# Performance work log

Measured on AMD Instinct MI355X. Metric: run time of the kernel, lower is better.

The kernel has to match this reference:

```python
import jax, jax.numpy as jnp
import numpy as np

RNN = 64      # rnn_hidden_dim
HID = 64      # hidden_dim
ENC = 3       # encoder_dim
NAG = 8       # n_agents
NACT = 14     # n_actions
CLIP = 0.2    # args.exp_clip (variance floor)
BN_EPS = 1e-5


def _bn(x, g, b):
    # BatchNorm1d in training mode: batch stats, biased variance
    m = x.mean(0)
    v = jnp.mean((x - m) ** 2, 0)
    return g * (x - m) * jax.lax.rsqrt(v + BN_EPS) + b


def setup_inputs() -> dict:
    key = jax.random.key(0)
    ks = jax.random.split(key, 16)
    B, INP = 8192, 96

    def w(k, shape, fan):
        return (jax.random.normal(k, shape, jnp.float32) / np.float32(np.sqrt(fan)))

    d = {}
    d["inputs"] = jax.random.normal(ks[0], (B * NAG, INP), jnp.float32)
    d["hidden_state"] = jax.random.normal(ks[1], (B * NAG, RNN), jnp.float32)
    d["noise"] = jax.random.normal(ks[2], (B, NAG, NAG * ENC), jnp.float32)
    d["fc1_w"] = w(ks[3], (INP, RNN), INP); d["fc1_b"] = jnp.zeros((RNN,), jnp.float32)
    d["w_ih"] = w(ks[4], (RNN, 3 * RNN), RNN); d["w_hh"] = w(ks[5], (RNN, 3 * RNN), RNN)
    d["b_ih"] = jnp.zeros((3 * RNN,), jnp.float32); d["b_hh"] = jnp.zeros((3 * RNN,), jnp.float32)
    d["aw1_w"] = w(ks[6], (RNN, HID), RNN); d["aw1_b"] = jnp.zeros((HID,), jnp.float32)
    d["aw_g"] = jnp.ones((HID,), jnp.float32); d["aw_be"] = jnp.zeros((HID,), jnp.float32)
    d["aw2_w"] = w(ks[7], (HID, 2 * NAG * ENC), HID); d["aw2_b"] = jnp.zeros((2 * NAG * ENC,), jnp.float32)
    d["po1_w"] = w(ks[8], (2 * RNN, HID), 2 * RNN); d["po1_b"] = jnp.zeros((HID,), jnp.float32)
    d["po_g"] = jnp.ones((HID,), jnp.float32); d["po_be"] = jnp.zeros((HID,), jnp.float32)
    d["po2_w"] = w(ks[9], (HID, 2 * ENC), HID); d["po2_b"] = jnp.zeros((2 * ENC,), jnp.float32)
    d["fc2_w"] = w(ks[10], (RNN + ENC * NAG, NACT), RNN + ENC * NAG); d["fc2_b"] = jnp.zeros((NACT,), jnp.float32)
    return d


def reference(inputs, hidden_state, noise,
              fc1_w, fc1_b, w_ih, w_hh, b_ih, b_hh,
              aw1_w, aw1_b, aw_g, aw_be, aw2_w, aw2_b,
              po1_w, po1_b, po_g, po_be, po2_w, po2_b,
              fc2_w, fc2_b):
    B, n, enc = noise.shape[0], NAG, ENC

    x = jax.nn.relu(inputs @ fc1_w + fc1_b)                      # [B*n, RNN]
    h_in = hidden_state.reshape(-1, RNN)

    # torch GRUCell
    gi = x @ w_ih + b_ih
    gh = h_in @ w_hh + b_hh
    ir, iz, i_n = jnp.split(gi, 3, axis=-1)
    hr, hz, h_n = jnp.split(gh, 3, axis=-1)
    r = jax.nn.sigmoid(ir + hr)
    z = jax.nn.sigmoid(iz + hz)
    nt = jnp.tanh(i_n + r * h_n)
    h = (1.0 - z) * nt + z * h_in                                # [B*n, RNN]

    # awareness encoder
    a = jax.nn.relu(_bn(h @ aw1_w + aw1_b, aw_g, aw_be))
    aw = (a @ aw2_w + aw2_b).reshape(B, n, 2 * n * enc)
    mu = aw[:, :, : n * enc]
    sigma = jnp.maximum(jnp.exp(aw[:, :, n * enc:]), CLIP)       # variance
    c = (mu + jnp.sqrt(sigma) * noise).reshape(-1, n * enc)      # rsample

    x_out = jnp.concatenate([h, c], axis=-1) @ fc2_w + fc2_b     # [B*n, NACT]

    # poster branch (training mode): all-pairs concat H[b, j, id] = [h[b,id], h[b,j]]
    hd = jax.lax.stop_gradient(h).reshape(B, n, RNN)
    Hi = jnp.broadcast_to(hd[:, None, :, :], (B, n, n, RNN))     # axis2 = id
    Hj = jnp.broadcast_to(hd[:, :, None, :], (B, n, n, RNN))     # axis1 = j
    H = jnp.concatenate([Hi, Hj], axis=-1).reshape(-1, 2 * RNN)  # [B*n*n, 2*RNN]

    p = jax.nn.relu(_bn(H @ po1_w + po1_b, po_g, po_be))
    out = (p @ po2_w + po2_b).reshape(B, n, 2 * n * enc)
    mu1 = out[:, :, : n * enc]
    sigma1 = jnp.maximum(jnp.exp(out[:, :, n * enc:]), CLIP)

    # KL between diagonal Gaussians (sigma, sigma1 are variances)
    kl = 0.5 * (jnp.log(sigma1 / sigma) + (sigma + (mu - mu1) ** 2) / sigma1 - 1.0)
    KL = kl.mean(axis=-1).mean(axis=-1, keepdims=True)           # [B, 1]
    return (x_out, h, KL)
```

## Files before the change

### kernel.cpp

```cpp
#include <hip/hip_runtime.h>
#include <math.h>

#define NROWS 65536
#define NB    8192
#define STAT_OFF  0
#define DERIV_OFF 448
#define WPACK_OFF 1088
#define OUT_XOUT 0
#define OUT_H    917504
#define OUT_KL   5111808

typedef __attribute__((ext_vector_type(8))) short bhalf8;
typedef __attribute__((ext_vector_type(4))) float floatx4;
typedef __attribute__((ext_vector_type(4))) unsigned short u16x4;

__device__ __forceinline__ float sigmf(float x) { return 1.0f / (1.0f + __expf(-x)); }
__device__ __forceinline__ float tanhfast(float x) {
    x = fminf(fmaxf(x, -15.f), 15.f);
    float e = __expf(-2.f * x);
    return (1.f - e) / (1.f + e);
}
__device__ __forceinline__ unsigned short f2bf(float f) {
    unsigned int u = __float_as_uint(f);
    u += 0x7FFFu + ((u >> 16) & 1u);
    return (unsigned short)(u >> 16);
}
__device__ __forceinline__ float bf2f(unsigned short s) {
    return __uint_as_float(((unsigned int)s) << 16);
}

__global__ void k_prep(const float* __restrict__ fc1_w,
                       const float* __restrict__ w_ih, const float* __restrict__ w_hh,
                       const float* __restrict__ aw1_w, const float* __restrict__ po1_w,
                       const float* __restrict__ aw2_w, const float* __restrict__ fc2_w,
                       float* __restrict__ ws)
{
    const int t = threadIdx.x;
    if (blockIdx.x == 0)
        for (int i = t; i < 448; i += 256) ws[STAT_OFF + i] = 0.f;

    unsigned short* wpk = (unsigned short*)(ws + WPACK_OFF);
    for (int f = blockIdx.x * 256 + t; f < 5952; f += gridDim.x * 256) {
        int lane, c, tile;
        const float* src;
        int colbase, krowstride, kofs, kmax = 1 << 30, colmax = 16;
        if (f < 768) {
            tile = f / 192; c = (f % 192) / 64; lane = f % 64;
            src = fc1_w; krowstride = 64; colbase = tile * 16; kofs = 0;
        } else if (f < 3840) {
            int f2 = f - 768;
            tile = f2 / 128; c = (f2 % 128) / 64; lane = f2 % 64;
            if (tile < 12) { src = w_ih; colbase = tile * 16; }
            else           { src = w_hh; colbase = (tile - 12) * 16; }
            krowstride = 192; kofs = 0;
        } else if (f < 5376) {
            int f3 = f - 3840;
            tile = f3 / 128; c = (f3 % 128) / 64; lane = f3 % 64;
            if (tile < 4)       { src = aw1_w; colbase = tile * 16; kofs = 0; }
            else if (tile < 8)  { src = po1_w; colbase = (tile - 4) * 16; kofs = 0; }
            else                { src = po1_w; colbase = (tile - 8) * 16; kofs = 64; }
            krowstride = 64;
        } else if (f < 5760) {
            int f4 = f - 5376;
            tile = f4 / 128; c = (f4 % 128) / 64; lane = f4 % 64;
            src = aw2_w; krowstride = 48; colbase = tile * 16; kofs = 0;
        } else {
            int f5 = f - 5760;
            c = f5 / 64; lane = f5 % 64;
            src = fc2_w; krowstride = 14; colbase = 0; kofs = 0;
            kmax = 88; colmax = 14;
        }
        int n = lane & 15, quad = lane >> 4;
        int col = colbase + n;
        unsigned short o[8];
        #pragma unroll
        for (int j = 0; j < 8; j++) {
            int k = c * 32 + quad * 8 + j + kofs;
            float v = (k < kmax && n < colmax) ? src[(size_t)k * krowstride + col] : 0.f;
            o[j] = f2bf(v);
        }
        u16x4 lo, hi;
        lo.x = o[0]; lo.y = o[1]; lo.z = o[2]; lo.w = o[3];
        hi.x = o[4]; hi.y = o[5]; hi.z = o[6]; hi.w = o[7];
        *(u16x4*)&wpk[f * 8]     = lo;
        *(u16x4*)&wpk[f * 8 + 4] = hi;
    }
}

__global__ __launch_bounds__(256) void k_front(
    const float* __restrict__ inp, const float* __restrict__ hin,
    const float* __restrict__ fc1_b,
    const float* __restrict__ b_ih, const float* __restrict__ b_hh,
    const float* __restrict__ aw1_b,
    float* __restrict__ h_out, float* __restrict__ ws)
{
    __shared__ __align__(16) unsigned short s_inpb[64 * 104];
    __shared__ __align__(16) unsigned short s_hinb[64 * 88];
    __shared__ __align__(16) unsigned short s_xb[64 * 88];
    __shared__ float s_stat[448];

    const int t = threadIdx.x;
    const int row0 = blockIdx.x * 64;
    const int lane = t & 63;
    const int w = t >> 6;
    const int n16 = lane & 15;
    const int quad = lane >> 4;
    const int mrow = w * 16 + n16;

    {
        const float* gi = inp + (size_t)row0 * 96;
        for (int i = t; i < 1536; i += 256) {
            int r = i / 24, c4 = (i - r * 24) * 4;
            float4 v = *(const float4*)&gi[r * 96 + c4];
            u16x4 p; p.x = f2bf(v.x); p.y = f2bf(v.y); p.z = f2bf(v.z); p.w = f2bf(v.w);
            *(u16x4*)&s_inpb[r * 104 + c4] = p;
        }
        const float* gh = hin + (size_t)row0 * 64;
        for (int i = t; i < 1024; i += 256) {
            int r = i >> 4, c4 = (i & 15) * 4;
            float4 v = *(const float4*)&gh[r * 64 + c4];
            u16x4 p; p.x = f2bf(v.x); p.y = f2bf(v.y); p.z = f2bf(v.z); p.w = f2bf(v.w);
            *(u16x4*)&s_hinb[r * 88 + c4] = p;
        }
    }
    for (int i = t; i < 448; i += 256) s_stat[i] = 0.f;
    __syncthreads();

    const bhalf8* wp1 = (const bhalf8*)((const unsigned short*)(ws + WPACK_OFF));
    const bhalf8* wp2 = wp1 + 768;
    const bhalf8* wp3 = wp1 + 3840;

    {
        bhalf8 ai0 = *(const bhalf8*)&s_inpb[mrow * 104 + 0  + quad * 8];
        bhalf8 ai1 = *(const bhalf8*)&s_inpb[mrow * 104 + 32 + quad * 8];
        bhalf8 ai2 = *(const bhalf8*)&s_inpb[mrow * 104 + 64 + quad * 8];
        #pragma unroll
        for (int g = 0; g < 4; g++) {
            floatx4 d = {0.f, 0.f, 0.f, 0.f};
            d = __builtin_amdgcn_mfma_f32_16x16x32_bf16(ai0, wp1[(g * 3 + 0) * 64 + lane], d, 0, 0, 0);
            d = __builtin_amdgcn_mfma_f32_16x16x32_bf16(ai1, wp1[(g * 3 + 1) * 64 + lane], d, 0, 0, 0);
            d = __builtin_amdgcn_mfma_f32_16x16x32_bf16(ai2, wp1[(g * 3 + 2) * 64 + lane], d, 0, 0, 0);
            int col = g * 16 + n16;
            float bb = fc1_b[col];
            #pragma unroll
            for (int q = 0; q < 4; q++) {
                float xv = fmaxf(d[q] + bb, 0.f);
                s_xb[(w * 16 + quad * 4 + q) * 88 + col] = f2bf(xv);
            }
        }
    }

    floatx4 gr[4], gz[4], gn[4], gh2[4];
    {
        bhalf8 ax0 = *(const bhalf8*)&s_xb[mrow * 88 + 0  + quad * 8];
        bhalf8 ax1 = *(const bhalf8*)&s_xb[mrow * 88 + 32 + quad * 8];
        bhalf8 ah0 = *(const bhalf8*)&s_hinb[mrow * 88 + 0  + quad * 8];
        bhalf8 ah1 = *(const bhalf8*)&s_hinb[mrow * 88 + 32 + quad * 8];
        #pragma unroll
        for (int g = 0; g < 4; g++) {
            floatx4 d = {0.f, 0.f, 0.f, 0.f};
            d = __builtin_amdgcn_mfma_f32_16x16x32_bf16(ax0, wp2[((0 + g) * 2 + 0) * 64 + lane], d, 0, 0, 0);
            d = __builtin_amdgcn_mfma_f32_16x16x32_bf16(ax1, wp2[((0 + g) * 2 + 1) * 64 + lane], d, 0, 0, 0);
            d = __builtin_amdgcn_mfma_f32_16x16x32_bf16(ah0, wp2[((12 + g) * 2 + 0) * 64 + lane], d, 0, 0, 0);
            d = __builtin_amdgcn_mfma_f32_16x16x32_bf16(ah1, wp2[((12 + g) * 2 + 1) * 64 + lane], d, 0, 0, 0);
            gr[g] = d;
            floatx4 e = {0.f, 0.f, 0.f, 0.f};
            e = __builtin_amdgcn_mfma_f32_16x16x32_bf16(ax0, wp2[((4 + g) * 2 + 0) * 64 + lane], e, 0, 0, 0);
            e = __builtin_amdgcn_mfma_f32_16x16x32_bf16(ax1, wp2[((4 + g) * 2 + 1) * 64 + lane], e, 0, 0, 0);
            e = __builtin_amdgcn_mfma_f32_16x16x32_bf16(ah0, wp2[((16 + g) * 2 + 0) * 64 + lane], e, 0, 0, 0);
            e = __builtin_amdgcn_mfma_f32_16x16x32_bf16(ah1, wp2[((16 + g) * 2 + 1) * 64 + lane], e, 0, 0, 0);
            gz[g] = e;
            floatx4 p = {0.f, 0.f, 0.f, 0.f};
            p = __builtin_amdgcn_mfma_f32_16x16x32_bf16(ax0, wp2[((8 + g) * 2 + 0) * 64 + lane], p, 0, 0, 0);
            p = __builtin_amdgcn_mfma_f32_16x16x32_bf16(ax1, wp2[((8 + g) * 2 + 1) * 64 + lane], p, 0, 0, 0);
            gn[g] = p;
            floatx4 s = {0.f, 0.f, 0.f, 0.f};
            s = __builtin_amdgcn_mfma_f32_16x16x32_bf16(ah0, wp2[((20 + g) * 2 + 0) * 64 + lane], s, 0, 0, 0);
            s = __builtin_amdgcn_mfma_f32_16x16x32_bf16(ah1, wp2[((20 + g) * 2 + 1) * 64 + lane], s, 0, 0, 0);
            gh2[g] = s;
        }
    }
    __syncthreads();

    unsigned short* s_hb = s_inpb;
    #pragma unroll
    for (int g = 0; g < 4; g++) {
        int col = g * 16 + n16;
        float br_ = b_ih[col] + b_hh[col];
        float bz_ = b_ih[64 + col] + b_hh[64 + col];
        float bin_ = b_ih[128 + col];
        float bhn_ = b_hh[128 + col];
        #pragma unroll
        for (int q = 0; q < 4; q++) {
            int lrow = w * 16 + quad * 4 + q;
            size_t grow = (size_t)(row0 + lrow);
            float r  = sigmf(gr[g][q] + br_);
            float z  = sigmf(gz[g][q] + bz_);
            float nt = tanhfast(gn[g][q] + bin_ + r * (gh2[g][q] + bhn_));
            float hp = hin[grow * 64 + col];
            float h  = (1.f - z) * nt + z * hp;
            h_out[grow * 64 + col] = h;
            s_hb[lrow * 88 + col] = f2bf(h);
        }
    }

    {
        bhalf8 ah0 = *(const bhalf8*)&s_hb[mrow * 88 + 0  + quad * 8];
        bhalf8 ah1 = *(const bhalf8*)&s_hb[mrow * 88 + 32 + quad * 8];
        floatx4 g3[12];
        #pragma unroll
        for (int tt = 0; tt < 12; tt++) {
            floatx4 d = {0.f, 0.f, 0.f, 0.f};
            d = __builtin_amdgcn_mfma_f32_16x16x32_bf16(ah0, wp3[(tt * 2 + 0) * 64 + lane], d, 0, 0, 0);
            d = __builtin_amdgcn_mfma_f32_16x16x32_bf16(ah1, wp3[(tt * 2 + 1) * 64 + lane], d, 0, 0, 0);
            g3[tt] = d;
        }
        #pragma unroll
        for (int g = 0; g < 4; g++) {
            int col = g * 16 + n16;
            float ab = aw1_b[col];
            float s1 = 0.f, s2 = 0.f;
            #pragma unroll
            for (int q = 0; q < 4; q++) {
                float v = g3[g][q] + ab;
                s1 += v; s2 += v * v;
            }
            float t1 = s1 + __shfl_xor(s1, 16, 64); t1 += __shfl_xor(t1, 32, 64);
            float t2 = s2 + __shfl_xor(s2, 16, 64); t2 += __shfl_xor(t2, 32, 64);
            if (quad == 0) {
                atomicAdd(&s_stat[col], t1);
                atomicAdd(&s_stat[64 + col], t2);
            }
        }
        #pragma unroll
        for (int g = 0; g < 4; g++) {
            int col = g * 16 + n16;
            float su = 0.f, suq = 0.f, sv = 0.f, svq = 0.f;
            #pragma unroll
            for (int q = 0; q < 4; q++) {
                float uv = g3[4 + g][q]; su += uv; suq += uv * uv;
                float vv = g3[8 + g][q]; sv += vv; svq += vv * vv;
            }
            float u8 = su + __shfl_xor(su, 16, 64);
            float v8 = sv + __shfl_xor(sv, 16, 64);
            if ((quad & 1) == 0)
                atomicAdd(&s_stat[384 + col], u8 * v8 * (1.f / 64.f));
            float su16 = u8 + __shfl_xor(u8, 32, 64);
            float sv16 = v8 + __shfl_xor(v8, 32, 64);
            float suq16 = suq + __shfl_xor(suq, 16, 64); suq16 += __shfl_xor(suq16, 32, 64);
            float svq16 = svq + __shfl_xor(svq, 16, 64); svq16 += __shfl_xor(svq16, 32, 64);
            if (quad == 0) {
                atomicAdd(&s_stat[128 + col], su16);
                atomicAdd(&s_stat[192 + col], suq16);
                atomicAdd(&s_stat[256 + col], sv16);
                atomicAdd(&s_stat[320 + col], svq16);
            }
        }
    }
    __syncthreads();
    if (t < 64) {
        float* gs = ws + STAT_OFF;
        #pragma unroll
        for (int q = 0; q < 7; q++)
            atomicAdd(&gs[q * 64 + t], s_stat[q * 64 + t]);
    }
}

__global__ void k_stats(const float* __restrict__ aw_g, const float* __restrict__ aw_be,
                        const float* __restrict__ po_g, const float* __restrict__ po_be,
                        const float* __restrict__ po1_b, const float* __restrict__ po2_w,
                        float* __restrict__ ws)
{
    const int t = threadIdx.x;
    const float* st = ws + STAT_OFF;
    float* dv = ws + DERIV_OFF;
    if (t < 64) {
        const float invN = 1.f / 65536.f;
        float am = st[t] * invN;
        float av = st[64 + t] * invN - am * am;
        float asc = aw_g[t] * rsqrtf(av + 1e-5f);
        dv[t] = asc;
        dv[64 + t] = aw_be[t] - asc * am;
        float Eu = st[128 + t] * invN;
        float vu = st[192 + t] * invN - Eu * Eu;
        float Ev = st[256 + t] * invN;
        float vv = st[320 + t] * invN - Ev * Ev;
        float cov = st[384 + t] * (1.f / 8192.f) - Eu * Ev;
        float my = Eu + Ev + po1_b[t];
        float vy = vu + vv + 2.f * cov;
        float psc = po_g[t] * rsqrtf(vy + 1e-5f);
        dv[128 + t] = psc;
        dv[192 + t] = po_be[t] + psc * (po1_b[t] - my);
    }
    for (int i = t; i < 384; i += 128) {
        int d = i >> 6, c = i & 63;
        dv[256 + i] = po2_w[c * 6 + d];
    }
}

__global__ __launch_bounds__(128) void k_heads(
    const float* __restrict__ h_glob, const float* __restrict__ noise,
    const float* __restrict__ aw1_b, const float* __restrict__ aw2_b,
    const float* __restrict__ fc2_b, const float* __restrict__ po2_b,
    const float* __restrict__ ws, float* __restrict__ out)
{
    __shared__ __align__(16) unsigned short s_hb[32 * 104];
    __shared__ __align__(16) unsigned short s_U[32 * 72];
    __shared__ __align__(16) unsigned short s_V[32 * 72];
    __shared__ float s_ms[32 * 48];
    __shared__ __align__(16) float s_u2[32 * 48];
    __shared__ float s_kl[32];

    const int t = threadIdx.x;
    const int row0 = blockIdx.x * 32;
    const int b0 = blockIdx.x * 4;
    const int lane = t & 63;
    const int w = t >> 6;
    const int n16 = lane & 15;
    const int quad = lane >> 4;
    const int mrow = w * 16 + n16;
    const float* dv = ws + DERIV_OFF;

    {
        const float* gh = h_glob + (size_t)row0 * 64;
        for (int i = t; i < 512; i += 128) {
            int r = i >> 4, c4 = (i & 15) * 4;
            float4 v = *(const float4*)&gh[r * 64 + c4];
            u16x4 p; p.x = f2bf(v.x); p.y = f2bf(v.y); p.z = f2bf(v.z); p.w = f2bf(v.w);
            *(u16x4*)&s_hb[r * 104 + c4] = p;
        }
        for (int i = t; i < 64; i += 128) {
            int r = i >> 1, c4 = 88 + (i & 1) * 4;
            u16x4 z; z.x = 0; z.y = 0; z.z = 0; z.w = 0;
            *(u16x4*)&s_hb[r * 104 + c4] = z;
        }
    }
    __syncthreads();

    const bhalf8* wp3  = ((const bhalf8*)((const unsigned short*)(ws + WPACK_OFF))) + 3840;
    const bhalf8* wpa2 = wp3 + 1536;
    const bhalf8* wpf2 = wpa2 + 384;
    unsigned short* s_ab = (unsigned short*)s_u2;

    {
        bhalf8 ah0 = *(const bhalf8*)&s_hb[mrow * 104 + 0  + quad * 8];
        bhalf8 ah1 = *(const bhalf8*)&s_hb[mrow * 104 + 32 + quad * 8];
        floatx4 g3[12];
        #pragma unroll
        for (int tt = 0; tt < 12; tt++) {
            floatx4 d = {0.f, 0.f, 0.f, 0.f};
            d = __builtin_amdgcn_mfma_f32_16x16x32_bf16(ah0, wp3[(tt * 2 + 0) * 64 + lane], d, 0, 0, 0);
            d = __builtin_amdgcn_mfma_f32_16x16x32_bf16(ah1, wp3[(tt * 2 + 1) * 64 + lane], d, 0, 0, 0);
            g3[tt] = d;
        }
        #pragma unroll
        for (int g = 0; g < 4; g++) {
            int col = g * 16 + n16;
            float ab = aw1_b[col];
            float sc = dv[col], sf = dv[64 + col];
            #pragma unroll
            for (int q = 0; q < 4; q++) {
                int lrow = w * 16 + quad * 4 + q;
                float a = fmaxf(sc * (g3[g][q] + ab) + sf, 0.f);
                s_ab[lrow * 72 + col] = f2bf(a);
                s_U[lrow * 72 + col] = f2bf(g3[4 + g][q]);
                s_V[lrow * 72 + col] = f2bf(g3[8 + g][q]);
            }
        }
    }
    __syncthreads();

    {
        bhalf8 aa0 = *(const bhalf8*)&s_ab[mrow * 72 + 0  + quad * 8];
        bhalf8 aa1 = *(const bhalf8*)&s_ab[mrow * 72 + 32 + quad * 8];
        #pragma unroll
        for (int g = 0; g < 3; g++) {
            floatx4 d = {0.f, 0.f, 0.f, 0.f};
            d = __builtin_amdgcn_mfma_f32_16x16x32_bf16(aa0, wpa2[(g * 2 + 0) * 64 + lane], d, 0, 0, 0);
            d = __builtin_amdgcn_mfma_f32_16x16x32_bf16(aa1, wpa2[(g * 2 + 1) * 64 + lane], d, 0, 0, 0);
            int col = g * 16 + n16;
            float bb = aw2_b[col];
            #pragma unroll
            for (int q = 0; q < 4; q++) {
                int lrow = w * 16 + quad * 4 + q;
                float v = d[q] + bb;
                s_ms[lrow * 48 + col] = (col < 24) ? v : fmaxf(__expf(v), 0.2f);
            }
        }
    }
    __syncthreads();

    for (int i = t; i < 768; i += 128) {
        int r = i / 24, m = i - r * 24;
        float c = s_ms[r * 48 + m] + sqrtf(s_ms[r * 48 + 24 + m]) * noise[(size_t)(row0 + r) * 24 + m];
        s_hb[r * 104 + 64 + m] = f2bf(c);
    }
    __syncthreads();

    {
        bhalf8 hc0 = *(const bhalf8*)&s_hb[mrow * 104 + 0  + quad * 8];
        bhalf8 hc1 = *(const bhalf8*)&s_hb[mrow * 104 + 32 + quad * 8];
        bhalf8 hc2 = *(const bhalf8*)&s_hb[mrow * 104 + 64 + quad * 8];
        floatx4 d = {0.f, 0.f, 0.f, 0.f};
        d = __builtin_amdgcn_mfma_f32_16x16x32_bf16(hc0, wpf2[0 * 64 + lane], d, 0, 0, 0);
        d = __builtin_amdgcn_mfma_f32_16x16x32_bf16(hc1, wpf2[1 * 64 + lane], d, 0, 0, 0);
        d = __builtin_amdgcn_mfma_f32_16x16x32_bf16(hc2, wpf2[2 * 64 + lane], d, 0, 0, 0);
        if (n16 < 14) {
            float bb = fc2_b[n16];
            float* xout = out + OUT_XOUT;
            #pragma unroll
            for (int q = 0; q < 4; q++) {
                size_t grow = (size_t)(row0 + w * 16 + quad * 4 + q);
                xout[grow * 14 + n16] = d[q] + bb;
            }
        }
    }
    __syncthreads();

    float* s_out = s_u2;
    {
        const float* psc = dv + 128;
        const float* psh = dv + 192;
        const float* p2t = dv + 256;
        const int bl = t >> 5;
        const int rem = t & 31;
        const int i_ = rem >> 2;
        const int j0 = (rem & 3) * 2;
        float acc[2][6];
        #pragma unroll
        for (int jj = 0; jj < 2; jj++)
            #pragma unroll
            for (int d = 0; d < 6; d++) acc[jj][d] = 0.f;

        for (int c = 0; c < 64; c += 4) {
            u16x4 vb = *(const u16x4*)&s_V[(bl * 8 + i_) * 72 + c];
            float vv[4] = {bf2f(vb.x), bf2f(vb.y), bf2f(vb.z), bf2f(vb.w)};
            float ps[4]; *(float4*)ps = *(const float4*)&psc[c];
            float pf[4]; *(float4*)pf = *(const float4*)&psh[c];
            float wv[6][4];
            #pragma unroll
            for (int d = 0; d < 6; d++) *(float4*)wv[d] = *(const float4*)&p2t[d * 64 + c];
            #pragma unroll
            for (int jj = 0; jj < 2; jj++) {
                u16x4 ub = *(const u16x4*)&s_U[(bl * 8 + j0 + jj) * 72 + c];
                float p[4];
                p[0] = fmaxf(ps[0] * (bf2f(ub.x) + vv[0]) + pf[0], 0.f);
                p[1] = fmaxf(ps[1] * (bf2f(ub.y) + vv[1]) + pf[1], 0.f);
                p[2] = fmaxf(ps[2] * (bf2f(ub.z) + vv[2]) + pf[2], 0.f);
                p[3] = fmaxf(ps[3] * (bf2f(ub.w) + vv[3]) + pf[3], 0.f);
                #pragma unroll
                for (int d = 0; d < 6; d++)
                    acc[jj][d] += p[0] * wv[d][0] + p[1] * wv[d][1] + p[2] * wv[d][2] + p[3] * wv[d][3];
            }
        }
        #pragma unroll
        for (int jj = 0; jj < 2; jj++)
            #pragma unroll
            for (int d = 0; d < 6; d++)
                s_out[(bl * 8 + i_) * 48 + (j0 + jj) * 6 + d] = acc[jj][d] + po2_b[d];
    }
    __syncthreads();

    if (t < 32) {
        float s = 0.f;
        #pragma unroll 4
        for (int m = 0; m < 24; m++) {
            float mu0 = s_ms[t * 48 + m];
            float sg0 = s_ms[t * 48 + 24 + m];
            float mu1 = s_out[t * 48 + m];
            float sg1 = fmaxf(__expf(s_out[t * 48 + 24 + m]), 0.2f);
            float d0 = mu0 - mu1;
            s += __logf(sg1 / sg0) + (sg0 + d0 * d0) / sg1 - 1.f;
        }
        s_kl[t] = s;
    }
    __syncthreads();
    if (t < 4) {
        float s = 0.f;
        #pragma unroll
        for (int i = 0; i < 8; i++) s += s_kl[t * 8 + i];
        out[OUT_KL + b0 + t] = s * (0.5f / 192.f);
    }
}

extern "C" void kernel_launch(void* const* d_in, const int* in_sizes, int n_in,
                              void* d_out, int out_size, void* d_ws, size_t ws_size,
                              hipStream_t stream)
{
    (void)in_sizes; (void)n_in; (void)out_size; (void)ws_size;
    const float* inp   = (const float*)d_in[0];
    const float* hin   = (const float*)d_in[1];
    const float* noise = (const float*)d_in[2];
    const float* fc1_w = (const float*)d_in[3];
    const float* fc1_b = (const float*)d_in[4];
    const float* w_ih  = (const float*)d_in[5];
    const float* w_hh  = (const float*)d_in[6];
    const float* b_ih  = (const float*)d_in[7];
    const float* b_hh  = (const float*)d_in[8];
    const float* aw1_w = (const float*)d_in[9];
    const float* aw1_b = (const float*)d_in[10];
    const float* aw_g  = (const float*)d_in[11];
    const float* aw_be = (const float*)d_in[12];
    const float* aw2_w = (const float*)d_in[13];
    const float* aw2_b = (const float*)d_in[14];
    const float* po1_w = (const float*)d_in[15];
    const float* po1_b = (const float*)d_in[16];
    const float* po_g  = (const float*)d_in[17];
    const float* po_be = (const float*)d_in[18];
    const float* po2_w = (const float*)d_in[19];
    const float* po2_b = (const float*)d_in[20];
    const float* fc2_w = (const float*)d_in[21];
    const float* fc2_b = (const float*)d_in[22];
    float* out = (float*)d_out;
    float* ws  = (float*)d_ws;

    hipLaunchKernelGGL(k_prep,  dim3(8),    dim3(256), 0, stream,
                       fc1_w, w_ih, w_hh, aw1_w, po1_w, aw2_w, fc2_w, ws);
    hipLaunchKernelGGL(k_front, dim3(1024), dim3(256), 0, stream,
                       inp, hin, fc1_b, b_ih, b_hh, aw1_b, out + OUT_H, ws);
    hipLaunchKernelGGL(k_stats, dim3(1),    dim3(128), 0, stream,
                       aw_g, aw_be, po_g, po_be, po1_b, po2_w, ws);
    hipLaunchKernelGGL(k_heads, dim3(2048), dim3(128), 0, stream,
                       out + OUT_H, noise, aw1_b, aw2_b, fc2_b, po2_b, ws, out);
}
```

Before: 211.5 us.

## Double rows per front block, fold stats kernel into heads, prescale U/V in fp32

k_front now handles 128 rows per block, so each wave computes two 16-row MFMA tiles that share every loaded weight fragment, which halves weight fragment loads per row and the number of blocks. The single-block k_stats launch is removed, and each k_heads block recomputes the BatchNorm-derived scale and shift into shared memory, saving a serialized launch at the cost of redundant per-block work. The poster U/V terms are stored in fp32 with the BN scale and shift already applied, which cuts multiply work in the all-pairs loop but enlarges shared memory. k_prep uses more blocks, and the per-tile stat reductions are merged to issue fewer shuffles and atomics.

```diff
diff --git a/kernel.cpp b/kernel.cpp
--- a/kernel.cpp
+++ b/kernel.cpp
@@ -4,8 +4,7 @@
 #define NROWS 65536
 #define NB    8192
 #define STAT_OFF  0
-#define DERIV_OFF 448
-#define WPACK_OFF 1088
+#define WPACK_OFF 448
 #define OUT_XOUT 0
 #define OUT_H    917504
 #define OUT_KL   5111808
@@ -25,9 +24,6 @@
     u += 0x7FFFu + ((u >> 16) & 1u);
     return (unsigned short)(u >> 16);
 }
-__device__ __forceinline__ float bf2f(unsigned short s) {
-    return __uint_as_float(((unsigned int)s) << 16);
-}
 
 __global__ void k_prep(const float* __restrict__ fc1_w,
                        const float* __restrict__ w_ih, const float* __restrict__ w_hh,
@@ -43,31 +39,31 @@
     for (int f = blockIdx.x * 256 + t; f < 5952; f += gridDim.x * 256) {
         int lane, c, tile;
         const float* src;
-        int colbase, krowstride, kofs, kmax = 1 << 30, colmax = 16;
+        int colbase, krowstride, kofs = 0, kmax = 1 << 30, colmax = 16;
         if (f < 768) {
             tile = f / 192; c = (f % 192) / 64; lane = f % 64;
-            src = fc1_w; krowstride = 64; colbase = tile * 16; kofs = 0;
+            src = fc1_w; krowstride = 64; colbase = tile * 16;
         } else if (f < 3840) {
             int f2 = f - 768;
             tile = f2 / 128; c = (f2 % 128) / 64; lane = f2 % 64;
             if (tile < 12) { src = w_ih; colbase = tile * 16; }
             else           { src = w_hh; colbase = (tile - 12) * 16; }
-            krowstride = 192; kofs = 0;
+            krowstride = 192;
         } else if (f < 5376) {
             int f3 = f - 3840;
             tile = f3 / 128; c = (f3 % 128) / 64; lane = f3 % 64;
-            if (tile < 4)       { src = aw1_w; colbase = tile * 16; kofs = 0; }
-            else if (tile < 8)  { src = po1_w; colbase = (tile - 4) * 16; kofs = 0; }
+            if (tile < 4)       { src = aw1_w; colbase = tile * 16; }
+            else if (tile < 8)  { src = po1_w; colbase = (tile - 4) * 16; }
             else                { src = po1_w; colbase = (tile - 8) * 16; kofs = 64; }
             krowstride = 64;
         } else if (f < 5760) {
             int f4 = f - 5376;
             tile = f4 / 128; c = (f4 % 128) / 64; lane = f4 % 64;
-            src = aw2_w; krowstride = 48; colbase = tile * 16; kofs = 0;
+            src = aw2_w; krowstride = 48; colbase = tile * 16;
         } else {
             int f5 = f - 5760;
             c = f5 / 64; lane = f5 % 64;
-            src = fc2_w; krowstride = 14; colbase = 0; kofs = 0;
+            src = fc2_w; krowstride = 14; colbase = 0;
             kmax = 88; colmax = 14;
         }
         int n = lane & 15, quad = lane >> 4;
@@ -87,36 +83,35 @@
     }
 }
 
-__global__ __launch_bounds__(256) void k_front(
+__global__ __launch_bounds__(256, 2) void k_front(
     const float* __restrict__ inp, const float* __restrict__ hin,
     const float* __restrict__ fc1_b,
     const float* __restrict__ b_ih, const float* __restrict__ b_hh,
     const float* __restrict__ aw1_b,
     float* __restrict__ h_out, float* __restrict__ ws)
 {
-    __shared__ __align__(16) unsigned short s_inpb[64 * 104];
-    __shared__ __align__(16) unsigned short s_hinb[64 * 88];
-    __shared__ __align__(16) unsigned short s_xb[64 * 88];
+    __shared__ __align__(16) unsigned short s_inpb[128 * 104];
+    __shared__ __align__(16) unsigned short s_hinb[128 * 88];
+    __shared__ __align__(16) unsigned short s_xb[128 * 88];
     __shared__ float s_stat[448];
 
     const int t = threadIdx.x;
-    const int row0 = blockIdx.x * 64;
+    const int row0 = blockIdx.x * 128;
     const int lane = t & 63;
     const int w = t >> 6;
     const int n16 = lane & 15;
     const int quad = lane >> 4;
-    const int mrow = w * 16 + n16;
 
     {
         const float* gi = inp + (size_t)row0 * 96;
-        for (int i = t; i < 1536; i += 256) {
+        for (int i = t; i < 3072; i += 256) {
             int r = i / 24, c4 = (i - r * 24) * 4;
             float4 v = *(const float4*)&gi[r * 96 + c4];
             u16x4 p; p.x = f2bf(v.x); p.y = f2bf(v.y); p.z = f2bf(v.z); p.w = f2bf(v.w);
             *(u16x4*)&s_inpb[r * 104 + c4] = p;
         }
         const float* gh = hin + (size_t)row0 * 64;
-        for (int i = t; i < 1024; i += 256) {
+        for (int i = t; i < 2048; i += 256) {
             int r = i >> 4, c4 = (i & 15) * 4;
             float4 v = *(const float4*)&gh[r * 64 + c4];
             u16x4 p; p.x = f2bf(v.x); p.y = f2bf(v.y); p.z = f2bf(v.z); p.w = f2bf(v.w);
@@ -131,53 +126,101 @@
     const bhalf8* wp3 = wp1 + 3840;
 
     {
-        bhalf8 ai0 = *(const bhalf8*)&s_inpb[mrow * 104 + 0  + quad * 8];
-        bhalf8 ai1 = *(const bhalf8*)&s_inpb[mrow * 104 + 32 + quad * 8];
-        bhalf8 ai2 = *(const bhalf8*)&s_inpb[mrow * 104 + 64 + quad * 8];
+        bhalf8 ai[2][3];
+        #pragma unroll
+        for (int u = 0; u < 2; u++) {
+            int mr = w * 32 + u * 16 + n16;
+            ai[u][0] = *(const bhalf8*)&s_inpb[mr * 104 + 0  + quad * 8];
+            ai[u][1] = *(const bhalf8*)&s_inpb[mr * 104 + 32 + quad * 8];
+            ai[u][2] = *(const bhalf8*)&s_inpb[mr * 104 + 64 + quad * 8];
+        }
         #pragma unroll
         for (int g = 0; g < 4; g++) {
-            floatx4 d = {0.f, 0.f, 0.f, 0.f};
-            d = __builtin_amdgcn_mfma_f32_16x16x32_bf16(ai0, wp1[(g * 3 + 0) * 64 + lane], d, 0, 0, 0);
-            d = __builtin_amdgcn_mfma_f32_16x16x32_bf16(ai1, wp1[(g * 3 + 1) * 64 + lane], d, 0, 0, 0);
-            d = __builtin_amdgcn_mfma_f32_16x16x32_bf16(ai2, wp1[(g * 3 + 2) * 64 + lane], d, 0, 0, 0);
+            bhalf8 f0 = wp1[(g * 3 + 0) * 64 + lane];
+            bhalf8 f1 = wp1[(g * 3 + 1) * 64 + lane];
+            bhalf8 f2 = wp1[(g * 3 + 2) * 64 + lane];
             int col = g * 16 + n16;
             float bb = fc1_b[col];
             #pragma unroll
-            for (int q = 0; q < 4; q++) {
-                float xv = fmaxf(d[q] + bb, 0.f);
-                s_xb[(w * 16 + quad * 4 + q) * 88 + col] = f2bf(xv);
-            }
-        }
-    }
-
-    floatx4 gr[4], gz[4], gn[4], gh2[4];
-    {
-        bhalf8 ax0 = *(const bhalf8*)&s_xb[mrow * 88 + 0  + quad * 8];
-        bhalf8 ax1 = *(const bhalf8*)&s_xb[mrow * 88 + 32 + quad * 8];
-        bhalf8 ah0 = *(const bhalf8*)&s_hinb[mrow * 88 + 0  + quad * 8];
-        bhalf8 ah1 = *(const bhalf8*)&s_hinb[mrow * 88 + 32 + quad * 8];
+            for (int u = 0; u < 2; u++) {
+                floatx4 d = {0.f, 0.f, 0.f, 0.f};
+                d = __builtin_amdgcn_mfma_f32_16x16x32_bf16(ai[u][0], f0, d, 0, 0, 0);
+                d = __builtin_amdgcn_mfma_f32_16x16x32_bf16(ai[u][1], f1, d, 0, 0, 0);
+                d = __builtin_amdgcn_mfma_f32_16x16x32_bf16(ai[u][2], f2, d, 0, 0, 0);
+                #pragma unroll
+                for (int q = 0; q < 4; q++) {
+                    float xv = fmaxf(d[q] + bb, 0.f);
+                    s_xb[(w * 32 + u * 16 + quad * 4 + q) * 88 + col] = f2bf(xv);
+                }
+            }
+        }
+    }
+
+    floatx4 gr[2][4], gz[2][4], gn[2][4], gh2[2][4];
+    {
+        bhalf8 ax0[2], ax1[2], ah0[2], ah1[2];
+        #pragma unroll
+        for (int u = 0; u < 2; u++) {
+            int mr = w * 32 + u * 16 + n16;
+            ax0[u] = *(const bhalf8*)&s_xb[mr * 88 + 0  + quad * 8];
+            ax1[u] = *(const bhalf8*)&s_xb[mr * 88 + 32 + quad * 8];
+            ah0[u] = *(const bhalf8*)&s_hinb[mr * 88 + 0  + quad * 8];
+            ah1[u] = *(const bhalf8*)&s_hinb[mr * 88 + 32 + quad * 8];
+        }
         #pragma unroll
         for (int g = 0; g < 4; g++) {
-            floatx4 d = {0.f, 0.f, 0.f, 0.f};
-            d = __builtin_amdgcn_mfma_f32_16x16x32_bf16(ax0, wp2[((0 + g) * 2 + 0) * 64 + lane], d, 0, 0, 0);
-            d = __builtin_amdgcn_mfma_f32_16x16x32_bf16(ax1, wp2[((0 + g) * 2 + 1) * 64 + lane], d, 0, 0, 0);
-            d = __builtin_amdgcn_mfma_f32_16x16x32_bf16(ah0, wp2[((12 + g) * 2 + 0) * 64 + lane], d, 0, 0, 0);
-            d = __builtin_amdgcn_mfma_f32_16x16x32_bf16(ah1, wp2[((12 + g) * 2 + 1) * 64 + lane], d, 0, 0, 0);
-            gr[g] = d;
-            floatx4 e = {0.f, 0.f, 0.f, 0.f};
-            e = __builtin_amdgcn_mfma_f32_16x16x32_bf16(ax0, wp2[((4 + g) * 2 + 0) * 64 + lane], e, 0, 0, 0);
-            e = __builtin_amdgcn_mfma_f32_16x16x32_bf16(ax1, wp2[((4 + g) * 2 + 1) * 64 + lane], e, 0, 0, 0);
-            e = __builtin_amdgcn_mfma_f32_16x16x32_bf16(ah0, wp2[((16 + g) * 2 + 0) * 64 + lane], e, 0, 0, 0);
-            e = __builtin_amdgcn_mfma_f32_16x16x32_bf16(ah1, wp2[((16 + g) * 2 + 1) * 64 + lane], e, 0, 0, 0);
-            gz[g] = e;
-            floatx4 p = {0.f, 0.f, 0.f, 0.f};
-            p = __builtin_amdgcn_mfma_f32_16x16x32_bf16(ax0, wp2[((8 + g) * 2 + 0) * 64 + lane], p, 0, 0, 0);
-            p = __builtin_amdgcn_mfma_f32_16x16x32_bf16(ax1, wp2[((8 + g) * 2 + 1) * 64 + lane], p, 0, 0, 0);
-            gn[g] = p;
-            floatx4 s = {0.f, 0.f, 0.f, 0.f};
-            s = __builtin_amdgcn_mfma_f32_16x16x32_bf16(ah0, wp2[((20 + g) * 2 + 0) * 64 + lane], s, 0, 0, 0);
-            s = __builtin_amdgcn_mfma_f32_16x16x32_bf16(ah1, wp2[((20 + g) * 2 + 1) * 64 + lane], s, 0, 0, 0);
-            gh2[g] = s;
+            {
+                bhalf8 f0 = wp2[((0 + g) * 2 + 0) * 64 + lane];
+                bhalf8 f1 = wp2[((0 + g) * 2 + 1) * 64 + lane];
+                bhalf8 f2 = wp2[((12 + g) * 2 + 0) * 64 + lane];
+                bhalf8 f3 = wp2[((12 + g) * 2 + 1) * 64 + lane];
+                #pragma unroll
+                for (int u = 0; u < 2; u++) {
+                    floatx4 d = {0.f, 0.f, 0.f, 0.f};
+                    d = __builtin_amdgcn_mfma_f32_16x16x32_bf16(ax0[u], f0, d, 0, 0, 0);
+                    d = __builtin_amdgcn_mfma_f32_16x16x32_bf16(ax1[u], f1, d, 0, 0, 0);
+                    d = __builtin_amdgcn_mfma_f32_16x16x32_bf16(ah0[u], f2, d, 0, 0, 0);
+                    d = __builtin_amdgcn_mfma_f32_16x16x32_bf16(ah1[u], f3, d, 0, 0, 0);
+                    gr[u][g] = d;
+                }
+            }
+            {
+                bhalf8 f0 = wp2[((4 + g) * 2 + 0) * 64 + lane];
+                bhalf8 f1 = wp2[((4 + g) * 2 + 1) * 64 + lane];
+                bhalf8 f2 = wp2[((16 + g) * 2 + 0) * 64 + lane];
+                bhalf8 f3 = wp2[((16 + g) * 2 + 1) * 64 + lane];
+                #pragma unroll
+                for (int u = 0; u < 2; u++) {
+                    floatx4 d = {0.f, 0.f, 0.f, 0.f};
+                    d = __builtin_amdgcn_mfma_f32_16x16x32_bf16(ax0[u], f0, d, 0, 0, 0);
+                    d = __builtin_amdgcn_mfma_f32_16x16x32_bf16(ax1[u], f1, d, 0, 0, 0);
+                    d = __builtin_amdgcn_mfma_f32_16x16x32_bf16(ah0[u], f2, d, 0, 0, 0);
+                    d = __builtin_amdgcn_mfma_f32_16x16x32_bf16(ah1[u], f3, d, 0, 0, 0);
+                    gz[u][g] = d;
+                }
+            }
+            {
+                bhalf8 f0 = wp2[((8 + g) * 2 + 0) * 64 + lane];
+                bhalf8 f1 = wp2[((8 + g) * 2 + 1) * 64 + lane];
+                #pragma unroll
+                for (int u = 0; u < 2; u++) {
+                    floatx4 d = {0.f, 0.f, 0.f, 0.f};
+                    d = __builtin_amdgcn_mfma_f32_16x16x32_bf16(ax0[u], f0, d, 0, 0, 0);
+                    d = __builtin_amdgcn_mfma_f32_16x16x32_bf16(ax1[u], f1, d, 0, 0, 0);
+                    gn[u][g] = d;
+                }
+            }
+            {
+                bhalf8 f0 = wp2[((20 + g) * 2 + 0) * 64 + lane];
+                bhalf8 f1 = wp2[((20 + g) * 2 + 1) * 64 + lane];
+                #pragma unroll
+                for (int u = 0; u < 2; u++) {
+                    floatx4 d = {0.f, 0.f, 0.f, 0.f};
+                    d = __builtin_amdgcn_mfma_f32_16x16x32_bf16(ah0[u], f0, d, 0, 0, 0);
+                    d = __builtin_amdgcn_mfma_f32_16x16x32_bf16(ah1[u], f1, d, 0, 0, 0);
+                    gh2[u][g] = d;
+                }
+            }
         }
     }
     __syncthreads();
@@ -191,69 +234,80 @@
         float bin_ = b_ih[128 + col];
         float bhn_ = b_hh[128 + col];
         #pragma unroll
-        for (int q = 0; q < 4; q++) {
-            int lrow = w * 16 + quad * 4 + q;
-            size_t grow = (size_t)(row0 + lrow);
-            float r  = sigmf(gr[g][q] + br_);
-            float z  = sigmf(gz[g][q] + bz_);
-            float nt = tanhfast(gn[g][q] + bin_ + r * (gh2[g][q] + bhn_));
-            float hp = hin[grow * 64 + col];
-            float h  = (1.f - z) * nt + z * hp;
-            h_out[grow * 64 + col] = h;
-            s_hb[lrow * 88 + col] = f2bf(h);
-        }
-    }
-
-    {
-        bhalf8 ah0 = *(const bhalf8*)&s_hb[mrow * 88 + 0  + quad * 8];
-        bhalf8 ah1 = *(const bhalf8*)&s_hb[mrow * 88 + 32 + quad * 8];
-        floatx4 g3[12];
+        for (int u = 0; u < 2; u++) {
+            #pragma unroll
+            for (int q = 0; q < 4; q++) {
+                int lrow = w * 32 + u * 16 + quad * 4 + q;
+                size_t grow = (size_t)(row0 + lrow);
+                float r  = sigmf(gr[u][g][q] + br_);
+                float z  = sigmf(gz[u][g][q] + bz_);
+                float nt = tanhfast(gn[u][g][q] + bin_ + r * (gh2[u][g][q] + bhn_));
+                float hp = hin[grow * 64 + col];
+                float h  = (1.f - z) * nt + z * hp;
+                h_out[grow * 64 + col] = h;
+                s_hb[lrow * 88 + col] = f2bf(h);
+            }
+        }
+    }
+
+    {
+        bhalf8 bh0[2], bh1[2];
+        #pragma unroll
+        for (int u = 0; u < 2; u++) {
+            int mr = w * 32 + u * 16 + n16;
+            bh0[u] = *(const bhalf8*)&s_hb[mr * 88 + 0  + quad * 8];
+            bh1[u] = *(const bhalf8*)&s_hb[mr * 88 + 32 + quad * 8];
+        }
+        floatx4 g3[2][12];
         #pragma unroll
         for (int tt = 0; tt < 12; tt++) {
-            floatx4 d = {0.f, 0.f, 0.f, 0.f};
-            d = __builtin_amdgcn_mfma_f32_16x16x32_bf16(ah0, wp3[(tt * 2 + 0) * 64 + lane], d, 0, 0, 0);
-            d = __builtin_amdgcn_mfma_f32_16x16x32_bf16(ah1, wp3[(tt * 2 + 1) * 64 + lane], d, 0, 0, 0);
-            g3[tt] = d;
+            bhalf8 f0 = wp3[(tt * 2 + 0) * 64 + lane];
+            bhalf8 f1 = wp3[(tt * 2 + 1) * 64 + lane];
+            #pragma unroll
+            for (int u = 0; u < 2; u++) {
+                floatx4 d = {0.f, 0.f, 0.f, 0.f};
+                d = __builtin_amdgcn_mfma_f32_16x16x32_bf16(bh0[u], f0, d, 0, 0, 0);
+                d = __builtin_amdgcn_mfma_f32_16x16x32_bf16(bh1[u], f1, d, 0, 0, 0);
+                g3[u][tt] = d;
+            }
         }
         #pragma unroll
         for (int g = 0; g < 4; g++) {
             int col = g * 16 + n16;
             float ab = aw1_b[col];
-            float s1 = 0.f, s2 = 0.f;
-            #pragma unroll
-            for (int q = 0; q < 4; q++) {
-                float v = g3[g][q] + ab;
-                s1 += v; s2 += v * v;
-            }
-            float t1 = s1 + __shfl_xor(s1, 16, 64); t1 += __shfl_xor(t1, 32, 64);
-            float t2 = s2 + __shfl_xor(s2, 16, 64); t2 += __shfl_xor(t2, 32, 64);
+            float s1 = 0.f, s2 = 0.f, suq = 0.f, svq = 0.f;
+            float su[2] = {0.f, 0.f}, sv[2] = {0.f, 0.f};
+            #pragma unroll
+            for (int u = 0; u < 2; u++) {
+                #pragma unroll
+                for (int q = 0; q < 4; q++) {
+                    float a = g3[u][g][q] + ab; s1 += a; s2 += a * a;
+                    float uv = g3[u][4 + g][q]; su[u] += uv; suq += uv * uv;
+                    float vv = g3[u][8 + g][q]; sv[u] += vv; svq += vv * vv;
+                }
+            }
+            #pragma unroll
+            for (int u = 0; u < 2; u++) {
+                float u8 = su[u] + __shfl_xor(su[u], 16, 64);
+                float v8 = sv[u] + __shfl_xor(sv[u], 16, 64);
+                if ((quad & 1) == 0)
+                    atomicAdd(&s_stat[384 + col], u8 * v8 * (1.f / 64.f));
+            }
+            float sut = su[0] + su[1];
+            float svt = sv[0] + sv[1];
+            float t1 = s1 + __shfl_xor(s1, 16, 64);  t1 += __shfl_xor(t1, 32, 64);
+            float t2 = s2 + __shfl_xor(s2, 16, 64);  t2 += __shfl_xor(t2, 32, 64);
+            float t3 = sut + __shfl_xor(sut, 16, 64); t3 += __shfl_xor(t3, 32, 64);
+            float t4 = suq + __shfl_xor(suq, 16, 64); t4 += __shfl_xor(t4, 32, 64);
+            float t5 = svt + __shfl_xor(svt, 16, 64); t5 += __shfl_xor(t5, 32, 64);
+            float t6 = svq + __shfl_xor(svq, 16, 64); t6 += __shfl_xor(t6, 32, 64);
             if (quad == 0) {
                 atomicAdd(&s_stat[col], t1);
                 atomicAdd(&s_stat[64 + col], t2);
-            }
-        }
-        #pragma unroll
-        for (int g = 0; g < 4; g++) {
-            int col = g * 16 + n16;
-            float su = 0.f, suq = 0.f, sv = 0.f, svq = 0.f;
-            #pragma unroll
-            for (int q = 0; q < 4; q++) {
-                float uv = g3[4 + g][q]; su += uv; suq += uv * uv;
-                float vv = g3[8 + g][q]; sv += vv; svq += vv * vv;
-            }
-            float u8 = su + __shfl_xor(su, 16, 64);
-            float v8 = sv + __shfl_xor(sv, 16, 64);
-            if ((quad & 1) == 0)
-                atomicAdd(&s_stat[384 + col], u8 * v8 * (1.f / 64.f));
-            float su16 = u8 + __shfl_xor(u8, 32, 64);
-            float sv16 = v8 + __shfl_xor(v8, 32, 64);
-            float suq16 = suq + __shfl_xor(suq, 16, 64); suq16 += __shfl_xor(suq16, 32, 64);
-            float svq16 = svq + __shfl_xor(svq, 16, 64); svq16 += __shfl_xor(svq16, 32, 64);
-            if (quad == 0) {
-                atomicAdd(&s_stat[128 + col], su16);
-                atomicAdd(&s_stat[192 + col], suq16);
-                atomicAdd(&s_stat[256 + col], sv16);
-                atomicAdd(&s_stat[320 + col], svq16);
+                atomicAdd(&s_stat[128 + col], t3);
+                atomicAdd(&s_stat[192 + col], t4);
+                atomicAdd(&s_stat[256 + col], t5);
+                atomicAdd(&s_stat[320 + col], t6);
             }
         }
     }
@@ -266,21 +320,40 @@
     }
 }
 
-__global__ void k_stats(const float* __restrict__ aw_g, const float* __restrict__ aw_be,
-                        const float* __restrict__ po_g, const float* __restrict__ po_be,
-                        const float* __restrict__ po1_b, const float* __restrict__ po2_w,
-                        float* __restrict__ ws)
+__global__ __launch_bounds__(128) void k_heads(
+    const float* __restrict__ h_glob, const float* __restrict__ noise,
+    const float* __restrict__ aw1_b, const float* __restrict__ aw2_b,
+    const float* __restrict__ fc2_b, const float* __restrict__ po2_b,
+    const float* __restrict__ aw_g, const float* __restrict__ aw_be,
+    const float* __restrict__ po_g, const float* __restrict__ po_be,
+    const float* __restrict__ po1_b, const float* __restrict__ po2_w,
+    const float* __restrict__ ws, float* __restrict__ out)
 {
+    __shared__ __align__(16) unsigned short s_hb[32 * 104];
+    __shared__ __align__(16) float s_Uf[32 * 68];
+    __shared__ __align__(16) float s_Vf[32 * 68];
+    __shared__ float s_ms[32 * 48];
+    __shared__ __align__(16) float s_u2[32 * 48];
+    __shared__ __align__(16) float s_dv[640];
+    __shared__ float s_kl[32];
+
     const int t = threadIdx.x;
-    const float* st = ws + STAT_OFF;
-    float* dv = ws + DERIV_OFF;
+    const int row0 = blockIdx.x * 32;
+    const int b0 = blockIdx.x * 4;
+    const int lane = t & 63;
+    const int w = t >> 6;
+    const int n16 = lane & 15;
+    const int quad = lane >> 4;
+    const int mrow = w * 16 + n16;
+
     if (t < 64) {
+        const float* st = ws + STAT_OFF;
         const float invN = 1.f / 65536.f;
         float am = st[t] * invN;
         float av = st[64 + t] * invN - am * am;
         float asc = aw_g[t] * rsqrtf(av + 1e-5f);
-        dv[t] = asc;
-        dv[64 + t] = aw_be[t] - asc * am;
+        s_dv[t] = asc;
+        s_dv[64 + t] = aw_be[t] - asc * am;
         float Eu = st[128 + t] * invN;
         float vu = st[192 + t] * invN - Eu * Eu;
         float Ev = st[256 + t] * invN;
@@ -289,37 +362,13 @@
         float my = Eu + Ev + po1_b[t];
         float vy = vu + vv + 2.f * cov;
         float psc = po_g[t] * rsqrtf(vy + 1e-5f);
-        dv[128 + t] = psc;
-        dv[192 + t] = po_be[t] + psc * (po1_b[t] - my);
+        s_dv[128 + t] = psc;
+        s_dv[192 + t] = po_be[t] + psc * (po1_b[t] - my);
     }
     for (int i = t; i < 384; i += 128) {
         int d = i >> 6, c = i & 63;
-        dv[256 + i] = po2_w[c * 6 + d];
-    }
-}
-
-__global__ __launch_bounds__(128) void k_heads(
-    const float* __restrict__ h_glob, const float* __restrict__ noise,
-    const float* __restrict__ aw1_b, const float* __restrict__ aw2_b,
-    const float* __restrict__ fc2_b, const float* __restrict__ po2_b,
-    const float* __restrict__ ws, float* __restrict__ out)
-{
-    __shared__ __align__(16) unsigned short s_hb[32 * 104];
-    __shared__ __align__(16) unsigned short s_U[32 * 72];
-    __shared__ __align__(16) unsigned short s_V[32 * 72];
-    __shared__ float s_ms[32 * 48];
-    __shared__ __align__(16) float s_u2[32 * 48];
-    __shared__ float s_kl[32];
-
-    const int t = threadIdx.x;
-    const int row0 = blockIdx.x * 32;
-    const int b0 = blockIdx.x * 4;
-    const int lane = t & 63;
-    const int w = t >> 6;
-    const int n16 = lane & 15;
-    const int quad = lane >> 4;
-    const int mrow = w * 16 + n16;
-    const float* dv = ws + DERIV_OFF;
+        s_dv[256 + i] = po2_w[c * 6 + d];
+    }
 
     {
         const float* gh = h_glob + (size_t)row0 * 64;
@@ -357,14 +406,15 @@
         for (int g = 0; g < 4; g++) {
             int col = g * 16 + n16;
             float ab = aw1_b[col];
-            float sc = dv[col], sf = dv[64 + col];
+            float asc = s_dv[col], ash = s_dv[64 + col];
+            float psc = s_dv[128 + col], psh = s_dv[192 + col];
             #pragma unroll
             for (int q = 0; q < 4; q++) {
                 int lrow = w * 16 + quad * 4 + q;
-                float a = fmaxf(sc * (g3[g][q] + ab) + sf, 0.f);
+                float a = fmaxf(asc * (g3[g][q] + ab) + ash, 0.f);
                 s_ab[lrow * 72 + col] = f2bf(a);
-                s_U[lrow * 72 + col] = f2bf(g3[4 + g][q]);
-                s_V[lrow * 72 + col] = f2bf(g3[8 + g][q]);
+                s_Uf[lrow * 68 + col] = psc * g3[4 + g][q];
+                s_Vf[lrow * 68 + col] = psc * g3[8 + g][q] + psh;
             }
         }
     }
@@ -419,9 +469,7 @@
 
     float* s_out = s_u2;
     {
-        const float* psc = dv + 128;
-        const float* psh = dv + 192;
-        const float* p2t = dv + 256;
+        const float* p2t = s_dv + 256;
         const int bl = t >> 5;
         const int rem = t & 31;
         const int i_ = rem >> 2;
@@ -433,21 +481,16 @@
             for (int d = 0; d < 6; d++) acc[jj][d] = 0.f;
 
         for (int c = 0; c < 64; c += 4) {
-            u16x4 vb = *(const u16x4*)&s_V[(bl * 8 + i_) * 72 + c];
-            float vv[4] = {bf2f(vb.x), bf2f(vb.y), bf2f(vb.z), bf2f(vb.w)};
-            float ps[4]; *(float4*)ps = *(const float4*)&psc[c];
-            float pf[4]; *(float4*)pf = *(const float4*)&psh[c];
+            float vv[4]; *(float4*)vv = *(const float4*)&s_Vf[(bl * 8 + i_) * 68 + c];
             float wv[6][4];
             #pragma unroll
             for (int d = 0; d < 6; d++) *(float4*)wv[d] = *(const float4*)&p2t[d * 64 + c];
             #pragma unroll
             for (int jj = 0; jj < 2; jj++) {
-                u16x4 ub = *(const u16x4*)&s_U[(bl * 8 + j0 + jj) * 72 + c];
+                float uu[4]; *(float4*)uu = *(const float4*)&s_Uf[(bl * 8 + j0 + jj) * 68 + c];
                 float p[4];
-                p[0] = fmaxf(ps[0] * (bf2f(ub.x) + vv[0]) + pf[0], 0.f);
-                p[1] = fmaxf(ps[1] * (bf2f(ub.y) + vv[1]) + pf[1], 0.f);
-                p[2] = fmaxf(ps[2] * (bf2f(ub.z) + vv[2]) + pf[2], 0.f);
-                p[3] = fmaxf(ps[3] * (bf2f(ub.w) + vv[3]) + pf[3], 0.f);
+                #pragma unroll
+                for (int q = 0; q < 4; q++) p[q] = fmaxf(uu[q] + vv[q], 0.f);
                 #pragma unroll
                 for (int d = 0; d < 6; d++)
                     acc[jj][d] += p[0] * wv[d][0] + p[1] * wv[d][1] + p[2] * wv[d][2] + p[3] * wv[d][3];
@@ -514,12 +557,11 @@
     float* out = (float*)d_out;
     float* ws  = (float*)d_ws;
 
-    hipLaunchKernelGGL(k_prep,  dim3(8),    dim3(256), 0, stream,
+    hipLaunchKernelGGL(k_prep,  dim3(24),   dim3(256), 0, stream,
                        fc1_w, w_ih, w_hh, aw1_w, po1_w, aw2_w, fc2_w, ws);
-    hipLaunchKernelGGL(k_front, dim3(1024), dim3(256), 0, stream,
+    hipLaunchKernelGGL(k_front, dim3(512),  dim3(256), 0, stream,
                        inp, hin, fc1_b, b_ih, b_hh, aw1_b, out + OUT_H, ws);
-    hipLaunchKernelGGL(k_stats, dim3(1),    dim3(128), 0, stream,
-                       aw_g, aw_be, po_g, po_be, po1_b, po2_w, ws);
     hipLaunchKernelGGL(k_heads, dim3(2048), dim3(128), 0, stream,
-                       out + OUT_H, noise, aw1_b, aw2_b, fc2_b, po2_b, ws, out);
+                       out + OUT_H, noise, aw1_b, aw2_b, fc2_b, po2_b,
+                       aw_g, aw_be, po_g, po_be, po1_b, po2_w, ws, out);
 }
```

After: 197.7 us. -6.5%, faster.
